# Kernel optimization log

Measured on AMD Instinct MI355X. Metric: run time of the kernel, lower is better.

Reference implementation:

```python
import jax, jax.numpy as jnp
import numpy as np

MIN_LEVEL, MAX_LEVEL = 2, 5

# pywt Wavelet('db4') analysis filters (dec_lo / dec_hi)
DEC_LO = np.array([-0.010597401784997278, 0.032883011666982945, 0.030841381835986965,
                   -0.18703481171888114, -0.02798376941698385, 0.6308807679295904,
                   0.7148465705525415, 0.23037781330885523])
DEC_HI = np.array([-0.23037781330885523, 0.7148465705525415, -0.6308807679295904,
                   -0.02798376941698385, 0.18703481171888114, 0.030841381835986965,
                   -0.032883011666982945, -0.010597401784997278])
# pytorch_wavelets time-reverses the filters and uses cross-correlation (F.conv),
# which is exactly what lax.conv_general_dilated computes.
H0 = jnp.asarray(DEC_LO[::-1].copy(), jnp.float32)
H1 = jnp.asarray(DEC_HI[::-1].copy(), jnp.float32)


def _afb1d(x):
    """One-level analysis filter bank, 'zero' padding mode (pytorch_wavelets afb1d).
    x: (N, 1, T) -> (lo, hi) each (N, 1, floor((T+L-1)/2))."""
    T = x.shape[-1]
    L = H0.shape[0]
    out = (T + L - 1) // 2          # pywt.dwt_coeff_len(T, L, 'zero')
    p = 2 * out - T                 # total pad; extra zero goes to the right if odd
    xp = jnp.pad(x, ((0, 0), (0, 0), (p // 2, p - p // 2)))
    k = jnp.stack([H0, H1])[:, None, :]          # (2, 1, L)
    lohi = jax.lax.conv_general_dilated(
        xp, k, window_strides=(2,), padding='VALID',
        dimension_numbers=('NCH', 'OIH', 'NCH'))
    return lohi[:, 0:1, :], lohi[:, 1:2, :]


def _decompose(x, levels):
    """Batched multi-level DWT cascade over all features at once; per-feature
    decomposition level selected afterwards via one-hot / masking (same math as
    the original per-feature Python loop)."""
    B, S, F = x.shape
    cur = jnp.transpose(x, (0, 2, 1)).reshape(B * F, 1, S)
    los, his = [], []
    for _ in range(MAX_LEVEL):
        lo, hi = _afb1d(cur)

        def to_bsf(a):
            # zero-pad coeffs up to seq_len, back to (B, S, F) layout
            a = jnp.pad(a, ((0, 0), (0, 0), (0, S - a.shape[-1])))
            return jnp.transpose(a.reshape(B, F, S), (0, 2, 1))

        los.append(to_bsf(lo))
        his.append(to_bsf(hi))
        cur = lo
    los = jnp.stack(los)   # (MAX_LEVEL, B, S, F) lowpass after level j+1
    his = jnp.stack(his)   # (MAX_LEVEL, B, S, F) detail at level j+1

    # approx for feature f = lowpass after `levels[f]` levels
    sel = jax.nn.one_hot(levels - 1, MAX_LEVEL, dtype=x.dtype)      # (F, MAX_LEVEL)
    approx = jnp.einsum('lbsf,fl->bsf', los, sel)
    # details[i] only populated for i < levels[f]
    mask = (jnp.arange(MAX_LEVEL)[:, None] < levels[None, :]).astype(x.dtype)  # (L, F)
    details = his * mask[:, None, None, :]
    high_freq = details.sum(axis=0)
    low_freq = approx
    return approx, details, high_freq, low_freq


def setup_inputs() -> dict:
    key = jax.random.key(0)
    k1, k2 = jax.random.split(key)
    x = jax.random.normal(k1, (32, 4096, 64), jnp.float32)
    complexity_scores = jax.random.uniform(k2, (64,), jnp.float32)
    return {"x": x, "complexity_scores": complexity_scores}


def reference(x, complexity_scores):
    # level_scaled = min_level + round(score * (max_level - min_level)); Python round
    # and jnp.round both use round-half-to-even.
    levels = MIN_LEVEL + jnp.round(
        complexity_scores * (MAX_LEVEL - MIN_LEVEL)).astype(jnp.int32)
    levels = jnp.clip(levels, MIN_LEVEL, MAX_LEVEL)   # (F,)
    return _decompose(x, levels)
```

## Files before the change

### kernel.cpp

```cpp
#include <hip/hip_runtime.h>


#define NB 32
#define NS 4096
#define NF 64
#define BSF (NB * NS * NF)
#define NF4 (NF / 4)

typedef float f4v __attribute__((ext_vector_type(4)));

__constant__ float c_h0[8] = {
     0.23037781330885523f,  0.7148465705525415f,   0.6308807679295904f,
    -0.02798376941698385f, -0.18703481171888114f,  0.030841381835986965f,
     0.032883011666982945f, -0.010597401784997278f};
__constant__ float c_h1[8] = {
    -0.010597401784997278f, -0.032883011666982945f, 0.030841381835986965f,
     0.18703481171888114f,  -0.02798376941698385f,  -0.6308807679295904f,
     0.7148465705525415f,   -0.23037781330885523f};

__device__ __forceinline__ int get_level(const float* __restrict__ scores, int f) {
    int lv = 2 + (int)rintf(scores[f] * 3.0f);
    return min(5, max(2, lv));
}

__global__ __launch_bounds__(256) void wl_mega(
    const f4v* __restrict__ x, f4v* __restrict__ out4,
    f4v* __restrict__ ws, const float* __restrict__ scores)
{
    __shared__ f4v lds[3840];
    f4v* const L1 = lds;
    f4v* const L2 = lds + 2592;
    f4v* const L3 = lds;
    f4v* const L4 = lds + 576;

    const int wg = blockIdx.x;
    const int b  = wg >> 5;
    const int ts = wg & 31;
    const int f4 = threadIdx.x & 15;
    const int rr = threadIdx.x >> 4;
    const int f0 = f4 * 4;
    const f4v z = {0.f, 0.f, 0.f, 0.f};

    const f4v* const xcol = x + (size_t)b * NS * NF4 + f4;
    f4v* const det1 = out4 + (size_t)1 * (BSF / 4);
    f4v* const det2 = out4 + (size_t)2 * (BSF / 4);
    f4v* const det3 = out4 + (size_t)3 * (BSF / 4);
    f4v* const det4 = out4 + (size_t)4 * (BSF / 4);
    f4v* const det5 = out4 + (size_t)5 * (BSF / 4);
    f4v* const lo2w = ws;
    f4v* const lo3w = lo2w + (size_t)NB * 1024 * NF4;
    f4v* const lo4w = lo3w + (size_t)NB * 512 * NF4;
    f4v* const lo5w = lo4w + (size_t)NB * 256 * NF4;

    int lv[4];
#pragma unroll
    for (int c = 0; c < 4; ++c) lv[c] = get_level(scores, f0 + c);

    const int a1 = 64 * ts - 45;
    const int a2 = 32 * ts - 21;
    const int a3 = 16 * ts - 9;
    const int a4 = 8 * ts - 3;

#pragma unroll
    for (int k = 0; k < 11; ++k) {
        int ro = rr + 16 * k;
        if (ro < 162) {
            int m = a1 + ro;
            if ((unsigned)m < 2048u) {
                f4v lo = z;
#pragma unroll
                for (int i = 0; i < 8; ++i) {
                    int mm = 2 * m - 3 + i;
                    if ((unsigned)mm < (unsigned)NS) lo += c_h0[i] * xcol[(size_t)mm * NF4];
                }
                L1[ro * 16 + f4] = lo;
            }
        }
    }
#pragma unroll
    for (int k = 0; k < 4; ++k) {
        int n = 64 * ts + rr + 16 * k;
        f4v hi = z;
#pragma unroll
        for (int i = 0; i < 8; ++i) {
            int mm = 2 * n - 3 + i;
            if ((unsigned)mm < (unsigned)NS) hi += c_h1[i] * xcol[(size_t)mm * NF4];
        }
        det1[(size_t)(b * NS + n) * NF4 + f4] = hi;
    }
    __syncthreads();

#pragma unroll
    for (int k = 0; k < 5; ++k) {
        int ro = rr + 16 * k;
        if (ro < 78) {
            int m = a2 + ro;
            if ((unsigned)m < 1024u) {
                f4v lo = z;
#pragma unroll
                for (int i = 0; i < 8; ++i) {
                    int mm = 2 * m - 3 + i;
                    f4v v = ((unsigned)mm < 2048u) ? L1[(mm - a1) * 16 + f4] : z;
                    lo += c_h0[i] * v;
                }
                L2[ro * 16 + f4] = lo;
            }
        }
    }
#pragma unroll
    for (int k = 0; k < 2; ++k) {
        int n = 32 * ts + rr + 16 * k;
        f4v hi = z;
#pragma unroll
        for (int i = 0; i < 8; ++i) {
            int mm = 2 * n - 3 + i;
            f4v v = ((unsigned)mm < 2048u) ? L1[(mm - a1) * 16 + f4] : z;
            hi += c_h1[i] * v;
        }
        det2[(size_t)(b * NS + n) * NF4 + f4] = hi;
    }
    __syncthreads();

#pragma unroll
    for (int k = 0; k < 3; ++k) {
        int ro = rr + 16 * k;
        if (ro < 36) {
            int m = a3 + ro;
            if ((unsigned)m < 512u) {
                f4v lo = z;
#pragma unroll
                for (int i = 0; i < 8; ++i) {
                    int mm = 2 * m - 3 + i;
                    f4v v = ((unsigned)mm < 1024u) ? L2[(mm - a2) * 16 + f4] : z;
                    lo += c_h0[i] * v;
                }
                L3[ro * 16 + f4] = lo;
            }
        }
    }
    {
        int n = 16 * ts + rr;
        f4v hi = z;
#pragma unroll
        for (int i = 0; i < 8; ++i) {
            int mm = 2 * n - 3 + i;
            f4v v = ((unsigned)mm < 1024u) ? L2[(mm - a2) * 16 + f4] : z;
            hi += c_h1[i] * v;
        }
#pragma unroll
        for (int c = 0; c < 4; ++c) if (lv[c] < 3) hi[c] = 0.f;
        det3[(size_t)(b * NS + n) * NF4 + f4] = hi;
    }
#pragma unroll
    for (int k = 0; k < 2; ++k) {
        int n = 32 * ts + rr + 16 * k;
        lo2w[(size_t)(b * 1024 + n) * NF4 + f4] = L2[(n - a2) * 16 + f4];
    }
    __syncthreads();

    if (rr < 15) {
        int m = a4 + rr;
        if ((unsigned)m < 256u) {
            f4v lo = z;
#pragma unroll
            for (int i = 0; i < 8; ++i) {
                int mm = 2 * m - 3 + i;
                f4v v = ((unsigned)mm < 512u) ? L3[(mm - a3) * 16 + f4] : z;
                lo += c_h0[i] * v;
            }
            L4[rr * 16 + f4] = lo;
        }
    }
    if (rr < 8) {
        int n = 8 * ts + rr;
        f4v hi = z;
#pragma unroll
        for (int i = 0; i < 8; ++i) {
            int mm = 2 * n - 3 + i;
            f4v v = ((unsigned)mm < 512u) ? L3[(mm - a3) * 16 + f4] : z;
            hi += c_h1[i] * v;
        }
#pragma unroll
        for (int c = 0; c < 4; ++c) if (lv[c] < 4) hi[c] = 0.f;
        det4[(size_t)(b * NS + n) * NF4 + f4] = hi;
    }
    {
        int n = 16 * ts + rr;
        lo3w[(size_t)(b * 512 + n) * NF4 + f4] = L3[(n - a3) * 16 + f4];
    }
    __syncthreads();

    if (rr < 8) {
        int n = 8 * ts + rr;
        lo4w[(size_t)(b * 256 + n) * NF4 + f4] = L4[(n - a4) * 16 + f4];
    }
    if (rr < 4) {
        int n = 4 * ts + rr;
        f4v lo = z, hi = z;
#pragma unroll
        for (int i = 0; i < 8; ++i) {
            int mm = 2 * n - 3 + i;
            f4v v = ((unsigned)mm < 256u) ? L4[(mm - a4) * 16 + f4] : z;
            lo += c_h0[i] * v;
            hi += c_h1[i] * v;
        }
        lo5w[(size_t)(b * 128 + n) * NF4 + f4] = lo;
        f4v d5;
#pragma unroll
        for (int c = 0; c < 4; ++c) d5[c] = (lv[c] >= 5) ? hi[c] : 0.f;
        det5[(size_t)(b * NS + n) * NF4 + f4] = d5;
    }
}

__global__ __launch_bounds__(256) void wl_final(
    const float* __restrict__ lo2s, const float* __restrict__ lo3s,
    const float* __restrict__ lo4s, const float* __restrict__ lo5s,
    f4v* __restrict__ out4, const float* __restrict__ scores)
{
    const int SZA = NB * 1024 * NF4;
    int t = blockIdx.x * 256 + threadIdx.x;

    f4v* const det1 = out4 + (size_t)1 * (BSF / 4);
    f4v* const det2 = out4 + (size_t)2 * (BSF / 4);
    f4v* const det3 = out4 + (size_t)3 * (BSF / 4);
    f4v* const det4 = out4 + (size_t)4 * (BSF / 4);
    f4v* const det5 = out4 + (size_t)5 * (BSF / 4);
    f4v* const high = out4 + (size_t)6 * (BSF / 4);
    f4v* const lowp = out4 + (size_t)7 * (BSF / 4);
    const f4v z = {0.f, 0.f, 0.f, 0.f};

    if (t < SZA) {
        int f4 = t & (NF4 - 1);
        int r = t >> 4;
        int n = r & 1023;
        int b = r >> 10;
        int f0 = f4 * 4;
        f4v av = z;
#pragma unroll
        for (int c = 0; c < 4; ++c) {
            int L = get_level(scores, f0 + c);
            float vv = 0.f;
            if (L == 2)      vv = lo2s[(size_t)(b * 1024 + n) * NF + f0 + c];
            else if (L == 3) { if (n < 512) vv = lo3s[(size_t)(b * 512 + n) * NF + f0 + c]; }
            else if (L == 4) { if (n < 256) vv = lo4s[(size_t)(b * 256 + n) * NF + f0 + c]; }
            else             { if (n < 128) vv = lo5s[(size_t)(b * 128 + n) * NF + f0 + c]; }
            av[c] = vv;
        }
        size_t o = (size_t)(b * NS + n) * NF4 + f4;
        __builtin_nontemporal_store(av, out4 + o);
        __builtin_nontemporal_store(av, lowp + o);
        return;
    }
    t -= SZA;
    {
        int f4 = t & (NF4 - 1);
        int r = t >> 4;
        int n = r & 2047;
        int b = r >> 11;
        size_t o = (size_t)(b * NS + n) * NF4 + f4;
        f4v acc = det1[o];
        if (n < 1024) acc += det2[o];
        if (n < 512)  acc += det3[o];
        if (n < 256)  acc += det4[o];
        if (n < 128)  acc += det5[o];
        __builtin_nontemporal_store(acc, high + o);
    }
}

extern "C" void kernel_launch(void* const* d_in, const int* in_sizes, int n_in,
                              void* d_out, int out_size, void* d_ws, size_t ws_size,
                              hipStream_t stream)
{
    const f4v* x        = (const f4v*)d_in[0];
    const float* scores = (const float*)d_in[1];
    f4v* out4 = (f4v*)d_out;
    f4v* ws   = (f4v*)d_ws;

    const float* lo2s = (const float*)ws;
    const float* lo3s = lo2s + (size_t)NB * 1024 * NF;
    const float* lo4s = lo3s + (size_t)NB * 512 * NF;
    const float* lo5s = lo4s + (size_t)NB * 256 * NF;

    dim3 block(256);
    wl_mega<<<dim3(NB * 32), block, 0, stream>>>(x, out4, ws, scores);
    wl_final<<<dim3((NB * 1024 * NF4 + NB * 2048 * NF4) / 256), block, 0, stream>>>(
        lo2s, lo3s, lo4s, lo5s, out4, scores);
}
```

Before: 303.8 us.

## Split level-1 DWT into a fully parallel kernel and move level-5 lowpass into final pass

Level 1 of the cascade moves out of the tiled mega kernel into its own fully parallel kernel. Each thread computes two adjacent lo/hi outputs from ten shared input loads and writes the level-1 lowpass to workspace. The cascade kernel then loads that lowpass into LDS instead of recomputing it with halo overlap from x, and uses simplified, bounds-free LDS indexing. The level-5 lowpass is now computed on demand in the final kernel from the level-4 workspace. This removes redundant halo recomputation and strided global reads, at the cost of an extra kernel launch and an extra workspace round trip for the level-1 lowpass.

```diff
diff --git a/kernel.cpp b/kernel.cpp
--- a/kernel.cpp
+++ b/kernel.cpp
@@ -23,199 +23,176 @@
     return min(5, max(2, lv));
 }
 
-__global__ __launch_bounds__(256) void wl_mega(
-    const f4v* __restrict__ x, f4v* __restrict__ out4,
+__global__ __launch_bounds__(256) void wl_l1(
+    const f4v* __restrict__ in, f4v* __restrict__ lo_out,
+    f4v* __restrict__ det)
+{
+    int t = blockIdx.x * 256 + threadIdx.x;
+    int f4 = t & (NF4 - 1);
+    int r = t >> 4;
+    int np = r & 1023;
+    int b = r >> 10;
+    int n0 = 2 * np;
+
+    const f4v* row = in + (size_t)b * NS * NF4 + f4;
+    const f4v z = {0.f, 0.f, 0.f, 0.f};
+    f4v v[10];
+    int base = n0 * 2 - 3;
+#pragma unroll
+    for (int j = 0; j < 10; ++j) {
+        int m = base + j;
+        v[j] = ((unsigned)m < (unsigned)NS) ? row[(size_t)m * NF4] : z;
+    }
+    f4v lo0 = z, hi0 = z, lo1v = z, hi1 = z;
+#pragma unroll
+    for (int i = 0; i < 8; ++i) {
+        lo0  += c_h0[i] * v[i];      hi0 += c_h1[i] * v[i];
+        lo1v += c_h0[i] * v[i + 2];  hi1 += c_h1[i] * v[i + 2];
+    }
+    f4v* lp = lo_out + (size_t)(b * 2048 + n0) * NF4 + f4;
+    lp[0] = lo0;  lp[NF4] = lo1v;
+    f4v* dp = det + (size_t)(b * NS + n0) * NF4 + f4;
+    dp[0] = hi0;  dp[NF4] = hi1;
+}
+
+__global__ __launch_bounds__(256) void wl_casc(
+    const f4v* __restrict__ lo1g, f4v* __restrict__ out4,
     f4v* __restrict__ ws, const float* __restrict__ scores)
 {
-    __shared__ f4v lds[3840];
+    __shared__ f4v lds[3648];
     f4v* const L1 = lds;
-    f4v* const L2 = lds + 2592;
+    f4v* const L2 = lds + 2464;
     f4v* const L3 = lds;
-    f4v* const L4 = lds + 576;
-
-    const int wg = blockIdx.x;
-    const int b  = wg >> 5;
-    const int ts = wg & 31;
+    f4v* const L4 = lds + 544;
+
+    const int b  = blockIdx.x >> 5;
+    const int ts = blockIdx.x & 31;
     const int f4 = threadIdx.x & 15;
-    const int rr = threadIdx.x >> 4;
+    const int rw = threadIdx.x >> 4;
     const int f0 = f4 * 4;
     const f4v z = {0.f, 0.f, 0.f, 0.f};
 
-    const f4v* const xcol = x + (size_t)b * NS * NF4 + f4;
-    f4v* const det1 = out4 + (size_t)1 * (BSF / 4);
+    int lv[4];
+#pragma unroll
+    for (int c = 0; c < 4; ++c) lv[c] = get_level(scores, f0 + c);
+
     f4v* const det2 = out4 + (size_t)2 * (BSF / 4);
     f4v* const det3 = out4 + (size_t)3 * (BSF / 4);
     f4v* const det4 = out4 + (size_t)4 * (BSF / 4);
     f4v* const det5 = out4 + (size_t)5 * (BSF / 4);
-    f4v* const lo2w = ws;
+    f4v* const lo2w = ws  + (size_t)NB * 2048 * NF4;
     f4v* const lo3w = lo2w + (size_t)NB * 1024 * NF4;
     f4v* const lo4w = lo3w + (size_t)NB * 512 * NF4;
-    f4v* const lo5w = lo4w + (size_t)NB * 256 * NF4;
-
-    int lv[4];
-#pragma unroll
-    for (int c = 0; c < 4; ++c) lv[c] = get_level(scores, f0 + c);
 
     const int a1 = 64 * ts - 45;
-    const int a2 = 32 * ts - 21;
-    const int a3 = 16 * ts - 9;
-    const int a4 = 8 * ts - 3;
-
-#pragma unroll
-    for (int k = 0; k < 11; ++k) {
-        int ro = rr + 16 * k;
-        if (ro < 162) {
+#pragma unroll
+    for (int k = 0; k < 10; ++k) {
+        int ro = rw + 16 * k;
+        if (ro < 154) {
             int m = a1 + ro;
-            if ((unsigned)m < 2048u) {
-                f4v lo = z;
-#pragma unroll
-                for (int i = 0; i < 8; ++i) {
-                    int mm = 2 * m - 3 + i;
-                    if ((unsigned)mm < (unsigned)NS) lo += c_h0[i] * xcol[(size_t)mm * NF4];
-                }
-                L1[ro * 16 + f4] = lo;
-            }
-        }
-    }
-#pragma unroll
-    for (int k = 0; k < 4; ++k) {
-        int n = 64 * ts + rr + 16 * k;
-        f4v hi = z;
-#pragma unroll
-        for (int i = 0; i < 8; ++i) {
-            int mm = 2 * n - 3 + i;
-            if ((unsigned)mm < (unsigned)NS) hi += c_h1[i] * xcol[(size_t)mm * NF4];
-        }
-        det1[(size_t)(b * NS + n) * NF4 + f4] = hi;
+            L1[ro * 16 + f4] = ((unsigned)m < 2048u)
+                ? lo1g[(size_t)(b * 2048 + m) * NF4 + f4] : z;
+        }
     }
     __syncthreads();
 
 #pragma unroll
     for (int k = 0; k < 5; ++k) {
-        int ro = rr + 16 * k;
-        if (ro < 78) {
-            int m = a2 + ro;
+        int ro = rw + 16 * k;
+        if (ro < 74) {
+            int m = 32 * ts - 21 + ro;
+            f4v lo = z;
             if ((unsigned)m < 1024u) {
-                f4v lo = z;
-#pragma unroll
-                for (int i = 0; i < 8; ++i) {
-                    int mm = 2 * m - 3 + i;
-                    f4v v = ((unsigned)mm < 2048u) ? L1[(mm - a1) * 16 + f4] : z;
-                    lo += c_h0[i] * v;
-                }
-                L2[ro * 16 + f4] = lo;
-            }
+#pragma unroll
+                for (int i = 0; i < 8; ++i)
+                    lo += c_h0[i] * L1[(2 * ro + i) * 16 + f4];
+            }
+            L2[ro * 16 + f4] = lo;
         }
     }
 #pragma unroll
     for (int k = 0; k < 2; ++k) {
-        int n = 32 * ts + rr + 16 * k;
-        f4v hi = z;
-#pragma unroll
-        for (int i = 0; i < 8; ++i) {
-            int mm = 2 * n - 3 + i;
-            f4v v = ((unsigned)mm < 2048u) ? L1[(mm - a1) * 16 + f4] : z;
-            hi += c_h1[i] * v;
-        }
-        det2[(size_t)(b * NS + n) * NF4 + f4] = hi;
+        int ro = rw + 16 * k;
+        f4v hi = z;
+#pragma unroll
+        for (int i = 0; i < 8; ++i)
+            hi += c_h1[i] * L1[(2 * ro + 42 + i) * 16 + f4];
+        det2[(size_t)(b * NS + 32 * ts + ro) * NF4 + f4] = hi;
     }
     __syncthreads();
 
 #pragma unroll
     for (int k = 0; k < 3; ++k) {
-        int ro = rr + 16 * k;
-        if (ro < 36) {
-            int m = a3 + ro;
+        int ro = rw + 16 * k;
+        if (ro < 34) {
+            int m = 16 * ts - 9 + ro;
+            f4v lo = z;
             if ((unsigned)m < 512u) {
-                f4v lo = z;
-#pragma unroll
-                for (int i = 0; i < 8; ++i) {
-                    int mm = 2 * m - 3 + i;
-                    f4v v = ((unsigned)mm < 1024u) ? L2[(mm - a2) * 16 + f4] : z;
-                    lo += c_h0[i] * v;
-                }
-                L3[ro * 16 + f4] = lo;
-            }
+#pragma unroll
+                for (int i = 0; i < 8; ++i)
+                    lo += c_h0[i] * L2[(2 * ro + i) * 16 + f4];
+            }
+            L3[ro * 16 + f4] = lo;
         }
     }
     {
-        int n = 16 * ts + rr;
-        f4v hi = z;
-#pragma unroll
-        for (int i = 0; i < 8; ++i) {
-            int mm = 2 * n - 3 + i;
-            f4v v = ((unsigned)mm < 1024u) ? L2[(mm - a2) * 16 + f4] : z;
-            hi += c_h1[i] * v;
-        }
+        f4v hi = z;
+#pragma unroll
+        for (int i = 0; i < 8; ++i)
+            hi += c_h1[i] * L2[(2 * rw + 18 + i) * 16 + f4];
 #pragma unroll
         for (int c = 0; c < 4; ++c) if (lv[c] < 3) hi[c] = 0.f;
-        det3[(size_t)(b * NS + n) * NF4 + f4] = hi;
+        det3[(size_t)(b * NS + 16 * ts + rw) * NF4 + f4] = hi;
     }
 #pragma unroll
     for (int k = 0; k < 2; ++k) {
-        int n = 32 * ts + rr + 16 * k;
-        lo2w[(size_t)(b * 1024 + n) * NF4 + f4] = L2[(n - a2) * 16 + f4];
-    }
-    __syncthreads();
-
-    if (rr < 15) {
-        int m = a4 + rr;
+        int ro = rw + 16 * k;
+        lo2w[(size_t)(b * 1024 + 32 * ts + ro) * NF4 + f4] =
+            L2[(ro + 21) * 16 + f4];
+    }
+    __syncthreads();
+
+    if (rw < 14) {
+        int m = 8 * ts - 3 + rw;
+        f4v lo = z;
         if ((unsigned)m < 256u) {
-            f4v lo = z;
-#pragma unroll
-            for (int i = 0; i < 8; ++i) {
-                int mm = 2 * m - 3 + i;
-                f4v v = ((unsigned)mm < 512u) ? L3[(mm - a3) * 16 + f4] : z;
-                lo += c_h0[i] * v;
-            }
-            L4[rr * 16 + f4] = lo;
-        }
-    }
-    if (rr < 8) {
-        int n = 8 * ts + rr;
-        f4v hi = z;
-#pragma unroll
-        for (int i = 0; i < 8; ++i) {
-            int mm = 2 * n - 3 + i;
-            f4v v = ((unsigned)mm < 512u) ? L3[(mm - a3) * 16 + f4] : z;
-            hi += c_h1[i] * v;
-        }
+#pragma unroll
+            for (int i = 0; i < 8; ++i)
+                lo += c_h0[i] * L3[(2 * rw + i) * 16 + f4];
+        }
+        L4[rw * 16 + f4] = lo;
+    }
+    if (rw < 8) {
+        f4v hi = z;
+#pragma unroll
+        for (int i = 0; i < 8; ++i)
+            hi += c_h1[i] * L3[(2 * rw + 6 + i) * 16 + f4];
 #pragma unroll
         for (int c = 0; c < 4; ++c) if (lv[c] < 4) hi[c] = 0.f;
-        det4[(size_t)(b * NS + n) * NF4 + f4] = hi;
-    }
-    {
-        int n = 16 * ts + rr;
-        lo3w[(size_t)(b * 512 + n) * NF4 + f4] = L3[(n - a3) * 16 + f4];
-    }
-    __syncthreads();
-
-    if (rr < 8) {
-        int n = 8 * ts + rr;
-        lo4w[(size_t)(b * 256 + n) * NF4 + f4] = L4[(n - a4) * 16 + f4];
-    }
-    if (rr < 4) {
-        int n = 4 * ts + rr;
-        f4v lo = z, hi = z;
-#pragma unroll
-        for (int i = 0; i < 8; ++i) {
-            int mm = 2 * n - 3 + i;
-            f4v v = ((unsigned)mm < 256u) ? L4[(mm - a4) * 16 + f4] : z;
-            lo += c_h0[i] * v;
-            hi += c_h1[i] * v;
-        }
-        lo5w[(size_t)(b * 128 + n) * NF4 + f4] = lo;
+        det4[(size_t)(b * NS + 8 * ts + rw) * NF4 + f4] = hi;
+    }
+    lo3w[(size_t)(b * 512 + 16 * ts + rw) * NF4 + f4] = L3[(rw + 9) * 16 + f4];
+    __syncthreads();
+
+    if (rw < 4) {
+        f4v hi = z;
+#pragma unroll
+        for (int i = 0; i < 8; ++i)
+            hi += c_h1[i] * L4[(2 * rw + i) * 16 + f4];
         f4v d5;
 #pragma unroll
         for (int c = 0; c < 4; ++c) d5[c] = (lv[c] >= 5) ? hi[c] : 0.f;
-        det5[(size_t)(b * NS + n) * NF4 + f4] = d5;
+        det5[(size_t)(b * NS + 4 * ts + rw) * NF4 + f4] = d5;
+    }
+    if (rw < 8) {
+        lo4w[(size_t)(b * 256 + 8 * ts + rw) * NF4 + f4] = L4[(rw + 3) * 16 + f4];
     }
 }
 
 __global__ __launch_bounds__(256) void wl_final(
     const float* __restrict__ lo2s, const float* __restrict__ lo3s,
-    const float* __restrict__ lo4s, const float* __restrict__ lo5s,
-    f4v* __restrict__ out4, const float* __restrict__ scores)
+    const float* __restrict__ lo4s, f4v* __restrict__ out4,
+    const float* __restrict__ scores)
 {
     const int SZA = NB * 1024 * NF4;
     int t = blockIdx.x * 256 + threadIdx.x;
@@ -235,15 +212,32 @@
         int n = r & 1023;
         int b = r >> 10;
         int f0 = f4 * 4;
+        int lv[4];
+#pragma unroll
+        for (int c = 0; c < 4; ++c) lv[c] = get_level(scores, f0 + c);
+
+        f4v l5 = z;
+        if (n < 128 && (lv[0] == 5 || lv[1] == 5 || lv[2] == 5 || lv[3] == 5)) {
+            const f4v* lo4row = (const f4v*)lo4s + (size_t)b * 256 * NF4 + f4;
+            int base = 2 * n - 3;
+#pragma unroll
+            for (int i = 0; i < 8; ++i) {
+                int m = base + i;
+                if ((unsigned)m < 256u) l5 += c_h0[i] * lo4row[(size_t)m * NF4];
+            }
+        }
         f4v av = z;
 #pragma unroll
         for (int c = 0; c < 4; ++c) {
-            int L = get_level(scores, f0 + c);
+            int L = lv[c];
+            int len = 2048 >> (L - 1);
             float vv = 0.f;
-            if (L == 2)      vv = lo2s[(size_t)(b * 1024 + n) * NF + f0 + c];
-            else if (L == 3) { if (n < 512) vv = lo3s[(size_t)(b * 512 + n) * NF + f0 + c]; }
-            else if (L == 4) { if (n < 256) vv = lo4s[(size_t)(b * 256 + n) * NF + f0 + c]; }
-            else             { if (n < 128) vv = lo5s[(size_t)(b * 128 + n) * NF + f0 + c]; }
+            if (n < len) {
+                if (L == 5)      vv = l5[c];
+                else if (L == 4) vv = lo4s[(size_t)(b * 256 + n) * NF + f0 + c];
+                else if (L == 3) vv = lo3s[(size_t)(b * 512 + n) * NF + f0 + c];
+                else             vv = lo2s[(size_t)(b * 1024 + n) * NF + f0 + c];
+            }
             av[c] = vv;
         }
         size_t o = (size_t)(b * NS + n) * NF4 + f4;
@@ -276,13 +270,16 @@
     f4v* out4 = (f4v*)d_out;
     f4v* ws   = (f4v*)d_ws;
 
-    const float* lo2s = (const float*)ws;
+    f4v* lo1 = ws;
+    const float* lo2s = (const float*)(ws + (size_t)NB * 2048 * NF4);
     const float* lo3s = lo2s + (size_t)NB * 1024 * NF;
     const float* lo4s = lo3s + (size_t)NB * 512 * NF;
-    const float* lo5s = lo4s + (size_t)NB * 256 * NF;
+
+    f4v* det1 = out4 + (size_t)1 * (BSF / 4);
 
     dim3 block(256);
-    wl_mega<<<dim3(NB * 32), block, 0, stream>>>(x, out4, ws, scores);
+    wl_l1<<<dim3(NB * 1024 * NF4 / 256), block, 0, stream>>>(x, lo1, det1);
+    wl_casc<<<dim3(NB * 32), block, 0, stream>>>(lo1, out4, ws, scores);
     wl_final<<<dim3((NB * 1024 * NF4 + NB * 2048 * NF4) / 256), block, 0, stream>>>(
-        lo2s, lo3s, lo4s, lo5s, out4, scores);
-}
+        lo2s, lo3s, lo4s, out4, scores);
+}
```

Measured after the change: 278.5 us. -8.3%, faster.
